# Kernel optimization log

Hardware: AMD Instinct MI355X
Metric: run time of the kernel (lower is better)

## Reference

```python
import jax, jax.numpy as jnp
import numpy as np

N = 50000        # num nodes
E = 800000       # num edges (before self loops)
IN = 256         # in_channels
H = 4            # heads
C = 32           # out_channels per head
NEG_SLOPE = 0.2


def _glorot(key, shape):
    fan = shape[-2] * (shape[-1] if len(shape) > 2 else 1) + shape[-1]
    # PyG glorot: uniform(-s, s) with s = sqrt(6 / (fan_in + fan_out))
    s = float(np.sqrt(6.0 / (shape[-2] + shape[-1])))
    return jax.random.uniform(key, shape, jnp.float32, -s, s)


def setup_inputs() -> dict:
    key = jax.random.key(0)
    k1, k2, k3, k4, k5 = jax.random.split(key, 5)
    x = jax.random.normal(k1, (N, IN), jnp.float32)
    src = jax.random.randint(k2, (E,), 0, N)
    dst = jax.random.randint(k3, (E,), 0, N)
    # guarantee no self loops (module removes them then re-adds exactly N loops)
    dst = jnp.where(dst == src, (dst + 1) % N, dst)
    edge_index = jnp.stack([src, dst]).astype(jnp.int32)
    weight = _glorot(k4, (IN, H * C))
    att = _glorot(k5, (1, H, 2 * C))
    bias = jnp.zeros((H * C,), jnp.float32)
    return {"x": x, "weight": weight, "att": att, "bias": bias,
            "edge_index": edge_index}


def reference(x, weight, att, bias, edge_index):
    n = x.shape[0]
    # linear projection -> [N, H, C]
    h = (x @ weight).reshape(n, H, C)
    # add self loops (input edge_index has none)
    loops = jnp.arange(n, dtype=edge_index.dtype)
    ei = jnp.concatenate([edge_index, jnp.stack([loops, loops])], axis=1)
    src, dst = ei[0], ei[1]          # flow source_to_target: j=src(row 0), i=dst(row 1)
    x_j = h[src]                     # [E', H, C] source features
    x_i = h[dst]                     # [E', H, C] target features
    wl = att[:, :, :C]               # applied to x_i (first half of concat)
    wr = att[:, :, C:]               # applied to x_j
    alpha = (x_i * wl).sum(-1) + (x_j * wr).sum(-1)   # [E', H]
    alpha = jax.nn.leaky_relu(alpha, NEG_SLOPE)
    # NOTE: module normalizes softmax over edge_index[0] (src) segments
    seg = src
    amax = jax.ops.segment_max(alpha, seg, num_segments=n)
    alpha = jnp.exp(alpha - amax[seg])
    denom = jax.ops.segment_sum(alpha, seg, num_segments=n)
    alpha = alpha / (denom[seg] + 1e-16)
    # weighted messages, aggregated at edge_index[i] = edge_index[1] (dst)
    msg = x_j * alpha[:, :, None]                     # [E', H, C]
    out = jax.ops.segment_sum(msg, dst, num_segments=n)  # [N, H, C]
    return out.reshape(n, H * C) + bias
```

## Files before the change

### kernel.cpp

```cpp
#include <hip/hip_runtime.h>
#include <hip/hip_fp16.h>
#include <math.h>


#define NH 4
#define CH 32
#define HC 128
#define IND 256
#define NEG_SLOPE 0.2f
#define CSH 8
#define NCB_MAX 256
#define CHUNK 4096

typedef __attribute__((ext_vector_type(8))) short bf16x8;
typedef __attribute__((ext_vector_type(16))) float f32x16;

__device__ __forceinline__ unsigned short f2bf(float f) {
    unsigned int u = __float_as_uint(f);
    unsigned int r = (u + 0x7FFFu + ((u >> 16) & 1u)) >> 16;
    return (unsigned short)r;
}
__device__ __forceinline__ float bf2f(unsigned short s) {
    return __uint_as_float(((unsigned int)s) << 16);
}

__global__ __launch_bounds__(256) void k_init0(int* __restrict__ histS,
                                               int* __restrict__ histD, int ncb) {
    int t = threadIdx.x;
    if (t < ncb) { histS[t] = 0; histD[t] = 0; }
}

__global__ __launch_bounds__(256) void k_wprep(const float* __restrict__ W,
                                               unsigned short* __restrict__ WT_bf) {
    int t = blockIdx.x * 256 + threadIdx.x;
    if (t >= IND * HC) return;
    int c = t >> 8;
    int k = t & 255;
    WT_bf[t] = f2bf(W[k * HC + c]);
}

__global__ __launch_bounds__(256) void k_gemm_mfma(const float* __restrict__ x,
                                                   const unsigned short* __restrict__ WT_bf,
                                                   const float* __restrict__ att,
                                                   unsigned short* __restrict__ h_bf,
                                                   float* __restrict__ al,
                                                   float* __restrict__ ar, int N) {
    __shared__ float cs[128 * 129];
    unsigned short* wsT = (unsigned short*)cs;

    const int tid  = threadIdx.x;
    const int row0 = blockIdx.x * 128;
    const int wave = tid >> 6;
    const int lane = tid & 63;
    const int n32  = lane & 31;
    const int half = lane >> 5;

    {
        int c  = tid >> 1;
        int kh = (tid & 1) * 128;
        const unsigned short* src = WT_bf + c * IND + kh;
        unsigned short* dst = wsT + c * 258 + kh;
#pragma unroll
        for (int j = 0; j < 128; j += 8)
            *(int4*)(dst + j) = *(const int4*)(src + j);
    }
    __syncthreads();

    const int row   = row0 + wave * 32 + n32;
    const bool valid = row < N;
    const float* xrow = x + (size_t)row * IND + half * 8;

    f32x16 acc[4];
#pragma unroll
    for (int t = 0; t < 4; t++)
#pragma unroll
        for (int r = 0; r < 16; r++) acc[t][r] = 0.0f;

#pragma unroll 4
    for (int s = 0; s < 16; s++) {
        float4 v0 = make_float4(0.f, 0.f, 0.f, 0.f);
        float4 v1 = v0;
        if (valid) {
            v0 = *(const float4*)(xrow + s * 16);
            v1 = *(const float4*)(xrow + s * 16 + 4);
        }
        bf16x8 a;
        a[0] = (short)f2bf(v0.x); a[1] = (short)f2bf(v0.y);
        a[2] = (short)f2bf(v0.z); a[3] = (short)f2bf(v0.w);
        a[4] = (short)f2bf(v1.x); a[5] = (short)f2bf(v1.y);
        a[6] = (short)f2bf(v1.z); a[7] = (short)f2bf(v1.w);
#pragma unroll
        for (int t = 0; t < 4; t++) {
            bf16x8 b = *(const bf16x8*)(wsT + (t * 32 + n32) * 258 + s * 16 + half * 8);
            acc[t] = __builtin_amdgcn_mfma_f32_32x32x16_bf16(a, b, acc[t], 0, 0, 0);
        }
    }
    __syncthreads();

#pragma unroll
    for (int t = 0; t < 4; t++)
#pragma unroll
        for (int r = 0; r < 16; r++) {
            int rl = wave * 32 + (r & 3) + 8 * (r >> 2) + 4 * half;
            cs[rl * 129 + t * 32 + n32] = acc[t][r];
        }
    __syncthreads();

    const int rl   = tid >> 1;
    const int chf  = tid & 1;
    const int orow = row0 + rl;
    if (orow < N) {
        const float* cr = cs + rl * 129 + chf * 64;
        unsigned short* hp = h_bf + (size_t)orow * HC + chf * 64;
#pragma unroll
        for (int c = 0; c < 64; c += 8) {
            ushort4 o0, o1;
            o0.x = f2bf(cr[c]);     o0.y = f2bf(cr[c + 1]);
            o0.z = f2bf(cr[c + 2]); o0.w = f2bf(cr[c + 3]);
            o1.x = f2bf(cr[c + 4]); o1.y = f2bf(cr[c + 5]);
            o1.z = f2bf(cr[c + 6]); o1.w = f2bf(cr[c + 7]);
            *(ushort4*)(hp + c) = o0;
            *(ushort4*)(hp + c + 4) = o1;
        }
        const int h0 = 2 * chf, h1 = 2 * chf + 1;
        const float* w0 = att + h0 * (2 * CH);
        const float* w1 = att + h1 * (2 * CH);
        float sl0 = 0.f, sr0 = 0.f, sl1 = 0.f, sr1 = 0.f;
#pragma unroll
        for (int c = 0; c < CH; c++) {
            float v0 = cr[c];
            float v1 = cr[CH + c];
            sl0 += v0 * w0[c];  sr0 += v0 * w0[CH + c];
            sl1 += v1 * w1[c];  sr1 += v1 * w1[CH + c];
        }
        al[orow * NH + h0] = sl0;  al[orow * NH + h1] = sl1;
        ar[orow * NH + h0] = sr0;  ar[orow * NH + h1] = sr1;
    }
}

__global__ __launch_bounds__(256) void k_hist(const int* __restrict__ ei,
                                              int* __restrict__ histS,
                                              int* __restrict__ histD,
                                              int E, int NE, int ncb) {
    __shared__ int hs[NCB_MAX], hd[NCB_MAX];
    hs[threadIdx.x] = 0; hd[threadIdx.x] = 0;
    __syncthreads();
    for (int t = blockIdx.x * 256 + threadIdx.x; t < NE; t += gridDim.x * 256) {
        int src, dst;
        if (t < E) { src = ei[t]; dst = ei[E + t]; }
        else       { src = dst = t - E; }
        atomicAdd(&hs[src >> CSH], 1);
        atomicAdd(&hd[dst >> CSH], 1);
    }
    __syncthreads();
    int i = threadIdx.x;
    if (i < ncb) {
        if (hs[i]) atomicAdd(&histS[i], hs[i]);
        if (hd[i]) atomicAdd(&histD[i], hd[i]);
    }
}

__global__ __launch_bounds__(256) void k_scanC(const int* __restrict__ histS,
                                               const int* __restrict__ histD,
                                               int* __restrict__ baseS,
                                               int* __restrict__ baseD,
                                               int* __restrict__ curS,
                                               int* __restrict__ curD,
                                               int* __restrict__ rowptrS,
                                               int* __restrict__ rowptrD,
                                               int ncb, int NE, int N) {
    __shared__ int sc[256];
    int tid = threadIdx.x;
    int v = (tid < ncb) ? histS[tid] : 0;
    sc[tid] = v;
    __syncthreads();
    for (int o = 1; o < 256; o <<= 1) {
        int t = (tid >= o) ? sc[tid - o] : 0;
        __syncthreads();
        sc[tid] += t;
        __syncthreads();
    }
    if (tid < ncb) { baseS[tid] = sc[tid] - v; curS[tid] = sc[tid] - v; }
    if (tid == 0) { baseS[ncb] = sc[255]; rowptrS[N] = NE; }
    __syncthreads();
    v = (tid < ncb) ? histD[tid] : 0;
    sc[tid] = v;
    __syncthreads();
    for (int o = 1; o < 256; o <<= 1) {
        int t = (tid >= o) ? sc[tid - o] : 0;
        __syncthreads();
        sc[tid] += t;
        __syncthreads();
    }
    if (tid < ncb) { baseD[tid] = sc[tid] - v; curD[tid] = sc[tid] - v; }
    if (tid == 0) { baseD[ncb] = sc[255]; rowptrD[N] = NE; }
}

__global__ __launch_bounds__(256) void k_scatterC(const int* __restrict__ ei,
                                                  int* __restrict__ gcurS,
                                                  int* __restrict__ gcurD,
                                                  unsigned int* __restrict__ recS,
                                                  unsigned int* __restrict__ recD,
                                                  int E, int NE, int ncb) {
    __shared__ unsigned int srt[CHUNK];
    __shared__ int cnt[NCB_MAX], off[NCB_MAX], cur[NCB_MAX], gpos[NCB_MAX], sc[256];
    const int tid = threadIdx.x;
    const int t0  = blockIdx.x * CHUNK;
    const int m   = min(CHUNK, NE - t0);

    unsigned int myrec[CHUNK / 256];
    int nmy = 0;
    for (int i = tid; i < m; i += 256) {
        int t = t0 + i;
        int src, dst;
        if (t < E) { src = ei[t]; dst = ei[E + t]; }
        else       { src = dst = t - E; }
        myrec[nmy++] = (unsigned int)src | ((unsigned int)dst << 16);
    }

    for (int side = 0; side < 2; side++) {
        cnt[tid] = 0;
        __syncthreads();
        int mybkt[CHUNK / 256];
        for (int k = 0; k < nmy; k++) {
            unsigned int r = myrec[k];
            int node = side ? (int)(r >> 16) : (int)(r & 0xFFFFu);
            mybkt[k] = node >> CSH;
            atomicAdd(&cnt[mybkt[k]], 1);
        }
        __syncthreads();
        int v = cnt[tid];
        sc[tid] = v;
        __syncthreads();
        for (int o = 1; o < 256; o <<= 1) {
            int t = (tid >= o) ? sc[tid - o] : 0;
            __syncthreads();
            sc[tid] += t;
            __syncthreads();
        }
        off[tid] = sc[tid] - v;
        cur[tid] = sc[tid] - v;
        __syncthreads();
        for (int k = 0; k < nmy; k++) {
            int p = atomicAdd(&cur[mybkt[k]], 1);
            srt[p] = myrec[k];
        }
        __syncthreads();
        int* gcur = side ? gcurD : gcurS;
        if (tid < ncb) {
            int c = cnt[tid];
            gpos[tid] = c ? atomicAdd(&gcur[tid], c) : 0;
        }
        __syncthreads();
        unsigned int* recX = side ? recD : recS;
        for (int i = tid; i < m; i += 256) {
            unsigned int r = srt[i];
            int node = side ? (int)(r >> 16) : (int)(r & 0xFFFFu);
            int cb = node >> CSH;
            recX[gpos[cb] + (i - off[cb])] = r;
        }
        __syncthreads();
    }
}

__global__ __launch_bounds__(256) void k_rebin(const unsigned int* __restrict__ recS,
                                               const unsigned int* __restrict__ recD,
                                               const int* __restrict__ baseS,
                                               const int* __restrict__ baseD,
                                               unsigned short* __restrict__ adjS,
                                               unsigned short* __restrict__ adjD,
                                               int* __restrict__ rowptrS,
                                               int* __restrict__ rowptrD,
                                               int ncb, int N) {
    __shared__ int cnt[256], cur[256], sc[256];
    const int tid  = threadIdx.x;
    const int side = (blockIdx.x >= ncb) ? 1 : 0;
    const int cb   = side ? blockIdx.x - ncb : blockIdx.x;
    const unsigned int* rec = side ? recD : recS;
    const int* base = side ? baseD : baseS;
    const int b0 = base[cb], b1 = base[cb + 1];
    const int tot_rec = b1 - b0;

    cnt[tid] = 0;
    __syncthreads();
    for (int i = tid; i < tot_rec; i += 256) {
        unsigned int r = rec[b0 + i];
        int node = side ? (int)(r >> 16) : (int)(r & 0xFFFFu);
        atomicAdd(&cnt[node & 255], 1);
    }
    __syncthreads();
    int v = cnt[tid];
    sc[tid] = v;
    __syncthreads();
    for (int o = 1; o < 256; o <<= 1) {
        int t = (tid >= o) ? sc[tid - o] : 0;
        __syncthreads();
        sc[tid] += t;
        __syncthreads();
    }
    int ex = sc[tid] - v;
    int node_g = (cb << CSH) + tid;
    int* rowptr = side ? rowptrD : rowptrS;
    if (node_g < N) rowptr[node_g] = b0 + ex;
    cur[tid] = ex;
    __syncthreads();
    unsigned short* adj = side ? adjD : adjS;
    for (int i = tid; i < tot_rec; i += 256) {
        unsigned int r = rec[b0 + i];
        int node = side ? (int)(r >> 16) : (int)(r & 0xFFFFu);
        unsigned short other = side ? (unsigned short)(r & 0xFFFFu)
                                    : (unsigned short)(r >> 16);
        int p = atomicAdd(&cur[node & 255], 1);
        adj[b0 + p] = other;
    }
}

__global__ __launch_bounds__(256) void k_denom(const int* __restrict__ rowptrS,
                                               const unsigned short* __restrict__ adjS,
                                               const float* __restrict__ al,
                                               const float* __restrict__ ar,
                                               float* __restrict__ rdenom, int N) {
    int n = blockIdx.x * 256 + threadIdx.x;
    if (n >= N) return;
    int beg = rowptrS[n], end = rowptrS[n + 1];
    float4 arv = *(const float4*)(ar + n * NH);
    float s0 = 0.f, s1 = 0.f, s2 = 0.f, s3 = 0.f;
    int i = beg;
    for (; i + 2 <= end; i += 2) {
        int d0 = adjS[i], d1 = adjS[i + 1];
        float4 av0 = *(const float4*)(al + d0 * NH);
        float4 av1 = *(const float4*)(al + d1 * NH);
        float a0 = av0.x + arv.x, a1 = av0.y + arv.y;
        float a2 = av0.z + arv.z, a3 = av0.w + arv.w;
        float c0 = av1.x + arv.x, c1 = av1.y + arv.y;
        float c2 = av1.z + arv.z, c3 = av1.w + arv.w;
        a0 = (a0 > 0.f) ? a0 : NEG_SLOPE * a0;
        a1 = (a1 > 0.f) ? a1 : NEG_SLOPE * a1;
        a2 = (a2 > 0.f) ? a2 : NEG_SLOPE * a2;
        a3 = (a3 > 0.f) ? a3 : NEG_SLOPE * a3;
        c0 = (c0 > 0.f) ? c0 : NEG_SLOPE * c0;
        c1 = (c1 > 0.f) ? c1 : NEG_SLOPE * c1;
        c2 = (c2 > 0.f) ? c2 : NEG_SLOPE * c2;
        c3 = (c3 > 0.f) ? c3 : NEG_SLOPE * c3;
        s0 += __expf(a0) + __expf(c0);
        s1 += __expf(a1) + __expf(c1);
        s2 += __expf(a2) + __expf(c2);
        s3 += __expf(a3) + __expf(c3);
    }
    if (i < end) {
        int d0 = adjS[i];
        float4 av = *(const float4*)(al + d0 * NH);
        float a0 = av.x + arv.x, a1 = av.y + arv.y;
        float a2 = av.z + arv.z, a3 = av.w + arv.w;
        a0 = (a0 > 0.f) ? a0 : NEG_SLOPE * a0;
        a1 = (a1 > 0.f) ? a1 : NEG_SLOPE * a1;
        a2 = (a2 > 0.f) ? a2 : NEG_SLOPE * a2;
        a3 = (a3 > 0.f) ? a3 : NEG_SLOPE * a3;
        s0 += __expf(a0); s1 += __expf(a1);
        s2 += __expf(a2); s3 += __expf(a3);
    }
    float4 r;
    r.x = 1.0f / (s0 + 1e-16f);
    r.y = 1.0f / (s1 + 1e-16f);
    r.z = 1.0f / (s2 + 1e-16f);
    r.w = 1.0f / (s3 + 1e-16f);
    *(float4*)(rdenom + n * NH) = r;
}

__global__ __launch_bounds__(256) void k_wedge(const int* __restrict__ rowptrD,
                                               const unsigned short* __restrict__ adjD,
                                               const float* __restrict__ al,
                                               const float* __restrict__ ar,
                                               const float* __restrict__ rdenom,
                                               unsigned short* __restrict__ wD, int N) {
    int n = blockIdx.x * 256 + threadIdx.x;
    if (n >= N) return;
    int beg = rowptrD[n], end = rowptrD[n + 1];
    float4 alv = *(const float4*)(al + n * NH);
    for (int i = beg; i < end; i++) {
        int s = adjD[i];
        float4 rv = *(const float4*)(ar + s * NH);
        float4 dv = *(const float4*)(rdenom + s * NH);
        float a0 = alv.x + rv.x, a1 = alv.y + rv.y;
        float a2 = alv.z + rv.z, a3 = alv.w + rv.w;
        a0 = (a0 > 0.f) ? a0 : NEG_SLOPE * a0;
        a1 = (a1 > 0.f) ? a1 : NEG_SLOPE * a1;
        a2 = (a2 > 0.f) ? a2 : NEG_SLOPE * a2;
        a3 = (a3 > 0.f) ? a3 : NEG_SLOPE * a3;
        ushort4 w;
        w.x = __half_as_ushort(__float2half(__expf(a0) * dv.x));
        w.y = __half_as_ushort(__float2half(__expf(a1) * dv.y));
        w.z = __half_as_ushort(__float2half(__expf(a2) * dv.z));
        w.w = __half_as_ushort(__float2half(__expf(a3) * dv.w));
        *(ushort4*)(wD + (size_t)i * NH) = w;
    }
}

__global__ __launch_bounds__(256) void k_agg(const int* __restrict__ rowptrD,
                                             const unsigned short* __restrict__ adjD,
                                             const unsigned short* __restrict__ wD,
                                             const unsigned short* __restrict__ h_bf,
                                             const float* __restrict__ bias,
                                             float* __restrict__ out, int N) {
    int n = blockIdx.x * 4 + (threadIdx.x >> 6);
    if (n >= N) return;
    int lane = threadIdx.x & 63;
    int c    = lane * 2;
    int hh   = lane >> 4;
    int beg = rowptrD[n], end = rowptrD[n + 1];
    float a0 = bias[c], a1 = bias[c + 1];
    float b0 = 0.f, b1 = 0.f;
    int i = beg;
    for (; i + 4 <= end; i += 4) {
        int s0 = adjD[i],     s1 = adjD[i + 1];
        int s2 = adjD[i + 2], s3 = adjD[i + 3];
        float w0 = __half2float(__ushort_as_half(wD[(size_t)i * NH + hh]));
        float w1 = __half2float(__ushort_as_half(wD[(size_t)(i + 1) * NH + hh]));
        float w2 = __half2float(__ushort_as_half(wD[(size_t)(i + 2) * NH + hh]));
        float w3 = __half2float(__ushort_as_half(wD[(size_t)(i + 3) * NH + hh]));
        ushort2 u0 = *(const ushort2*)(h_bf + (size_t)s0 * HC + c);
        ushort2 u1 = *(const ushort2*)(h_bf + (size_t)s1 * HC + c);
        ushort2 u2 = *(const ushort2*)(h_bf + (size_t)s2 * HC + c);
        ushort2 u3 = *(const ushort2*)(h_bf + (size_t)s3 * HC + c);
        a0 += bf2f(u0.x) * w0;  a1 += bf2f(u0.y) * w0;
        b0 += bf2f(u1.x) * w1;  b1 += bf2f(u1.y) * w1;
        a0 += bf2f(u2.x) * w2;  a1 += bf2f(u2.y) * w2;
        b0 += bf2f(u3.x) * w3;  b1 += bf2f(u3.y) * w3;
    }
    for (; i < end; i++) {
        int s0 = adjD[i];
        float w0 = __half2float(__ushort_as_half(wD[(size_t)i * NH + hh]));
        ushort2 u0 = *(const ushort2*)(h_bf + (size_t)s0 * HC + c);
        a0 += bf2f(u0.x) * w0;
        a1 += bf2f(u0.y) * w0;
    }
    *(float2*)(out + (size_t)n * HC + c) = make_float2(a0 + b0, a1 + b1);
}

extern "C" void kernel_launch(void* const* d_in, const int* in_sizes, int n_in,
                              void* d_out, int out_size, void* d_ws, size_t ws_size,
                              hipStream_t stream) {
    const float* x    = (const float*)d_in[0];
    const float* W    = (const float*)d_in[1];
    const float* att  = (const float*)d_in[2];
    const float* bias = (const float*)d_in[3];
    const int*   ei   = (const int*)d_in[4];

    const int N  = in_sizes[0] / IND;
    const int E  = in_sizes[4] / 2;
    const int NE = E + N;
    const int ncb = (N + (1 << CSH) - 1) >> CSH;
    float* out = (float*)d_out;
    const int nodeTot = N * NH;

    unsigned short* h_bf  = (unsigned short*)d_ws;
    unsigned short* WT_bf = h_bf + (size_t)N * HC;
    float* al      = (float*)(WT_bf + IND * HC);
    float* ar      = al + nodeTot;
    float* rdenom  = ar + nodeTot;
    unsigned int* recS = (unsigned int*)(rdenom + nodeTot);
    unsigned int* recD = recS + NE;
    unsigned short* adjS = (unsigned short*)(recD + NE);
    unsigned short* adjD = adjS + NE;
    unsigned short* wD   = adjD + NE + (NE & 1);
    int* rowptrS = (int*)(wD + (size_t)NE * NH);
    int* rowptrD = rowptrS + (N + 2);
    int* histS   = rowptrD + (N + 2);
    int* histD   = histS + NCB_MAX;
    int* baseS   = histD + NCB_MAX;
    int* baseD   = baseS + (NCB_MAX + 1);
    int* curS    = baseD + (NCB_MAX + 1);
    int* curD    = curS + NCB_MAX;

    k_init0<<<1, 256, 0, stream>>>(histS, histD, ncb);
    k_wprep<<<(IND * HC + 255) / 256, 256, 0, stream>>>(W, WT_bf);
    k_gemm_mfma<<<(N + 127) / 128, 256, 0, stream>>>(x, WT_bf, att, h_bf, al, ar, N);
    k_hist<<<256, 256, 0, stream>>>(ei, histS, histD, E, NE, ncb);
    k_scanC<<<1, 256, 0, stream>>>(histS, histD, baseS, baseD, curS, curD,
                                   rowptrS, rowptrD, ncb, NE, N);
    k_scatterC<<<(NE + CHUNK - 1) / CHUNK, 256, 0, stream>>>(ei, curS, curD,
                                                             recS, recD, E, NE, ncb);
    k_rebin<<<2 * ncb, 256, 0, stream>>>(recS, recD, baseS, baseD, adjS, adjD,
                                         rowptrS, rowptrD, ncb, N);
    k_denom<<<(N + 255) / 256, 256, 0, stream>>>(rowptrS, adjS, al, ar, rdenom, N);
    k_wedge<<<(N + 255) / 256, 256, 0, stream>>>(rowptrD, adjD, al, ar, rdenom, wD, N);
    k_agg<<<(N + 3) / 4, 256, 0, stream>>>(rowptrD, adjD, wD, h_bf, bias, out, N);
}
```

Measured before the change: 242.9 us.

## Fuse edge-weight computation into aggregation and pack ar with reciprocal denominators

Removes the separate k_wedge pass, which wrote per-edge fp16 softmax weights, and recomputes those weights inside k_agg from al[dst] and a packed per-node (ar, 1/denom) array written by k_denom. The aggregation now uses 32-lane groups, each covering 8 nodes per block. Each group loads 32 adjacency entries at a time and broadcasts them with shuffles, and each lane reads ushort4 feature chunks. This drops one kernel launch and a write-then-read of an E×4 weight buffer. In exchange, every lane recomputes exp, duplicated across the 8 lanes of each head.

After: 225.7 us. 7.1% less time.

```diff
diff --git a/kernel.cpp b/kernel.cpp
--- a/kernel.cpp
+++ b/kernel.cpp
@@ -319,7 +319,7 @@
                                                const unsigned short* __restrict__ adjS,
                                                const float* __restrict__ al,
                                                const float* __restrict__ ar,
-                                               float* __restrict__ rdenom, int N) {
+                                               float* __restrict__ arw, int N) {
     int n = blockIdx.x * 256 + threadIdx.x;
     if (n >= N) return;
     int beg = rowptrS[n], end = rowptrS[n + 1];
@@ -359,82 +359,82 @@
         s0 += __expf(a0); s1 += __expf(a1);
         s2 += __expf(a2); s3 += __expf(a3);
     }
-    float4 r;
-    r.x = 1.0f / (s0 + 1e-16f);
-    r.y = 1.0f / (s1 + 1e-16f);
-    r.z = 1.0f / (s2 + 1e-16f);
-    r.w = 1.0f / (s3 + 1e-16f);
-    *(float4*)(rdenom + n * NH) = r;
-}
-
-__global__ __launch_bounds__(256) void k_wedge(const int* __restrict__ rowptrD,
-                                               const unsigned short* __restrict__ adjD,
-                                               const float* __restrict__ al,
-                                               const float* __restrict__ ar,
-                                               const float* __restrict__ rdenom,
-                                               unsigned short* __restrict__ wD, int N) {
-    int n = blockIdx.x * 256 + threadIdx.x;
-    if (n >= N) return;
-    int beg = rowptrD[n], end = rowptrD[n + 1];
-    float4 alv = *(const float4*)(al + n * NH);
-    for (int i = beg; i < end; i++) {
-        int s = adjD[i];
-        float4 rv = *(const float4*)(ar + s * NH);
-        float4 dv = *(const float4*)(rdenom + s * NH);
-        float a0 = alv.x + rv.x, a1 = alv.y + rv.y;
-        float a2 = alv.z + rv.z, a3 = alv.w + rv.w;
-        a0 = (a0 > 0.f) ? a0 : NEG_SLOPE * a0;
-        a1 = (a1 > 0.f) ? a1 : NEG_SLOPE * a1;
-        a2 = (a2 > 0.f) ? a2 : NEG_SLOPE * a2;
-        a3 = (a3 > 0.f) ? a3 : NEG_SLOPE * a3;
-        ushort4 w;
-        w.x = __half_as_ushort(__float2half(__expf(a0) * dv.x));
-        w.y = __half_as_ushort(__float2half(__expf(a1) * dv.y));
-        w.z = __half_as_ushort(__float2half(__expf(a2) * dv.z));
-        w.w = __half_as_ushort(__float2half(__expf(a3) * dv.w));
-        *(ushort4*)(wD + (size_t)i * NH) = w;
-    }
+    float r0 = 1.0f / (s0 + 1e-16f);
+    float r1 = 1.0f / (s1 + 1e-16f);
+    float r2 = 1.0f / (s2 + 1e-16f);
+    float r3 = 1.0f / (s3 + 1e-16f);
+    float4 p0 = make_float4(arv.x, r0, arv.y, r1);
+    float4 p1 = make_float4(arv.z, r2, arv.w, r3);
+    *(float4*)(arw + (size_t)n * 8)     = p0;
+    *(float4*)(arw + (size_t)n * 8 + 4) = p1;
 }
 
 __global__ __launch_bounds__(256) void k_agg(const int* __restrict__ rowptrD,
                                              const unsigned short* __restrict__ adjD,
-                                             const unsigned short* __restrict__ wD,
+                                             const float* __restrict__ al,
+                                             const float* __restrict__ arw,
                                              const unsigned short* __restrict__ h_bf,
                                              const float* __restrict__ bias,
                                              float* __restrict__ out, int N) {
-    int n = blockIdx.x * 4 + (threadIdx.x >> 6);
+    const int g = threadIdx.x >> 5;
+    const int n = blockIdx.x * 8 + g;
     if (n >= N) return;
-    int lane = threadIdx.x & 63;
-    int c    = lane * 2;
-    int hh   = lane >> 4;
-    int beg = rowptrD[n], end = rowptrD[n + 1];
-    float a0 = bias[c], a1 = bias[c + 1];
-    float b0 = 0.f, b1 = 0.f;
-    int i = beg;
-    for (; i + 4 <= end; i += 4) {
-        int s0 = adjD[i],     s1 = adjD[i + 1];
-        int s2 = adjD[i + 2], s3 = adjD[i + 3];
-        float w0 = __half2float(__ushort_as_half(wD[(size_t)i * NH + hh]));
-        float w1 = __half2float(__ushort_as_half(wD[(size_t)(i + 1) * NH + hh]));
-        float w2 = __half2float(__ushort_as_half(wD[(size_t)(i + 2) * NH + hh]));
-        float w3 = __half2float(__ushort_as_half(wD[(size_t)(i + 3) * NH + hh]));
-        ushort2 u0 = *(const ushort2*)(h_bf + (size_t)s0 * HC + c);
-        ushort2 u1 = *(const ushort2*)(h_bf + (size_t)s1 * HC + c);
-        ushort2 u2 = *(const ushort2*)(h_bf + (size_t)s2 * HC + c);
-        ushort2 u3 = *(const ushort2*)(h_bf + (size_t)s3 * HC + c);
-        a0 += bf2f(u0.x) * w0;  a1 += bf2f(u0.y) * w0;
-        b0 += bf2f(u1.x) * w1;  b1 += bf2f(u1.y) * w1;
-        a0 += bf2f(u2.x) * w2;  a1 += bf2f(u2.y) * w2;
-        b0 += bf2f(u3.x) * w3;  b1 += bf2f(u3.y) * w3;
-    }
-    for (; i < end; i++) {
-        int s0 = adjD[i];
-        float w0 = __half2float(__ushort_as_half(wD[(size_t)i * NH + hh]));
-        ushort2 u0 = *(const ushort2*)(h_bf + (size_t)s0 * HC + c);
-        a0 += bf2f(u0.x) * w0;
-        a1 += bf2f(u0.y) * w0;
-    }
-    *(float2*)(out + (size_t)n * HC + c) = make_float2(a0 + b0, a1 + b1);
+    const int l  = threadIdx.x & 31;
+    const int c0 = l * 4;
+    const int hh = l >> 3;
+    const int beg = rowptrD[n], end = rowptrD[n + 1];
+    const float alv = al[n * NH + hh];
+
+    float a0 = 0.f, a1 = 0.f, a2 = 0.f, a3 = 0.f;
+
+    for (int base = beg; base < end; base += 32) {
+        int idx = base + l;
+        int av  = (idx < end) ? (int)adjD[idx] : 0;
+        int cnt = min(32, end - base);
+        int e = 0;
+        for (; e + 4 <= cnt; e += 4) {
+            int s0 = __shfl(av, e,     32);
+            int s1 = __shfl(av, e + 1, 32);
+            int s2 = __shfl(av, e + 2, 32);
+            int s3 = __shfl(av, e + 3, 32);
+            ushort4 u0 = *(const ushort4*)(h_bf + (size_t)s0 * HC + c0);
+            ushort4 u1 = *(const ushort4*)(h_bf + (size_t)s1 * HC + c0);
+            ushort4 u2 = *(const ushort4*)(h_bf + (size_t)s2 * HC + c0);
+            ushort4 u3 = *(const ushort4*)(h_bf + (size_t)s3 * HC + c0);
+            float2 p0 = *(const float2*)(arw + (size_t)s0 * 8 + hh * 2);
+            float2 p1 = *(const float2*)(arw + (size_t)s1 * 8 + hh * 2);
+            float2 p2 = *(const float2*)(arw + (size_t)s2 * 8 + hh * 2);
+            float2 p3 = *(const float2*)(arw + (size_t)s3 * 8 + hh * 2);
+            float t0 = alv + p0.x; t0 = (t0 > 0.f) ? t0 : NEG_SLOPE * t0;
+            float t1 = alv + p1.x; t1 = (t1 > 0.f) ? t1 : NEG_SLOPE * t1;
+            float t2 = alv + p2.x; t2 = (t2 > 0.f) ? t2 : NEG_SLOPE * t2;
+            float t3 = alv + p3.x; t3 = (t3 > 0.f) ? t3 : NEG_SLOPE * t3;
+            float w0 = __expf(t0) * p0.y;
+            float w1 = __expf(t1) * p1.y;
+            float w2 = __expf(t2) * p2.y;
+            float w3 = __expf(t3) * p3.y;
+            a0 += bf2f(u0.x) * w0; a1 += bf2f(u0.y) * w0;
+            a2 += bf2f(u0.z) * w0; a3 += bf2f(u0.w) * w0;
+            a0 += bf2f(u1.x) * w1; a1 += bf2f(u1.y) * w1;
+            a2 += bf2f(u1.z) * w1; a3 += bf2f(u1.w) * w1;
+            a0 += bf2f(u2.x) * w2; a1 += bf2f(u2.y) * w2;
+            a2 += bf2f(u2.z) * w2; a3 += bf2f(u2.w) * w2;
+            a0 += bf2f(u3.x) * w3; a1 += bf2f(u3.y) * w3;
+            a2 += bf2f(u3.z) * w3; a3 += bf2f(u3.w) * w3;
+        }
+        for (; e < cnt; e++) {
+            int s0 = __shfl(av, e, 32);
+            ushort4 u0 = *(const ushort4*)(h_bf + (size_t)s0 * HC + c0);
+            float2 p0 = *(const float2*)(arw + (size_t)s0 * 8 + hh * 2);
+            float t0 = alv + p0.x; t0 = (t0 > 0.f) ? t0 : NEG_SLOPE * t0;
+            float w0 = __expf(t0) * p0.y;
+            a0 += bf2f(u0.x) * w0; a1 += bf2f(u0.y) * w0;
+            a2 += bf2f(u0.z) * w0; a3 += bf2f(u0.w) * w0;
+        }
+    }
+    float4 b4 = *(const float4*)(bias + c0);
+    *(float4*)(out + (size_t)n * HC + c0) =
+        make_float4(a0 + b4.x, a1 + b4.y, a2 + b4.z, a3 + b4.w);
 }
 
 extern "C" void kernel_launch(void* const* d_in, const int* in_sizes, int n_in,
@@ -471,6 +471,7 @@
     int* baseD   = baseS + (NCB_MAX + 1);
     int* curS    = baseD + (NCB_MAX + 1);
     int* curD    = curS + NCB_MAX;
+    float* arw = (float*)((((uintptr_t)(curD + NCB_MAX)) + 255) & ~(uintptr_t)255);
 
     k_init0<<<1, 256, 0, stream>>>(histS, histD, ncb);
     k_wprep<<<(IND * HC + 255) / 256, 256, 0, stream>>>(W, WT_bf);
@@ -482,7 +483,6 @@
                                                              recS, recD, E, NE, ncb);
     k_rebin<<<2 * ncb, 256, 0, stream>>>(recS, recD, baseS, baseD, adjS, adjD,
                                          rowptrS, rowptrD, ncb, N);
-    k_denom<<<(N + 255) / 256, 256, 0, stream>>>(rowptrS, adjS, al, ar, rdenom, N);
-    k_wedge<<<(N + 255) / 256, 256, 0, stream>>>(rowptrD, adjD, al, ar, rdenom, wD, N);
-    k_agg<<<(N + 3) / 4, 256, 0, stream>>>(rowptrD, adjD, wD, h_bf, bias, out, N);
-}
+    k_denom<<<(N + 255) / 256, 256, 0, stream>>>(rowptrS, adjS, al, ar, arw, N);
+    k_agg<<<(N + 7) / 8, 256, 0, stream>>>(rowptrD, adjD, al, arw, h_bf, bias, out, N);
+}
```
